# Kernel optimization log

Hardware: AMD Instinct MI355X
Metric: run time of the kernel (lower is better)

## Reference

```python
import jax, jax.numpy as jnp
import numpy as np

NH, HD, WS, LL, SR, HF = 8, 32, 3, 9, 8, 682


def _ln(x, w, b, eps=1e-5):
    m = x.mean(-1, keepdims=True)
    v = ((x - m) ** 2).mean(-1, keepdims=True)
    return (x - m) * jax.lax.rsqrt(v + eps) * w + b


def _l2norm(x, eps=1e-12):
    n = jnp.sqrt(jnp.sum(x * x, axis=-1, keepdims=True))
    return x / jnp.maximum(n, eps)


def setup_inputs() -> dict:
    key = jax.random.key(0)
    ks = jax.random.split(key, 32)
    f32 = jnp.float32
    rn = lambda i, shp, s=0.02: jax.random.normal(ks[i], shp, f32) * s
    B, N, C, T = 8, 3136, 256, 1024
    d = {}
    d['x'] = jax.random.normal(ks[0], (B, N, C), f32)
    d['relative_coords_table'] = jax.random.uniform(ks[1], (T, 2), f32, minval=-1.0, maxval=1.0)
    d['seq_length_scale'] = jnp.ones((1,), f32)
    d['norm1_w'] = jnp.ones((C,), f32); d['norm1_b'] = jnp.zeros((C,), f32)
    d['q_w'] = rn(2, (C, C)); d['q_b'] = rn(3, (C,))
    d['kv_w'] = rn(4, (2 * C, C)); d['kv_b'] = rn(5, (2 * C,))
    d['temperature'] = jnp.full((NH, 1, 1), np.log(np.expm1(1.0 / 0.24)), f32)
    d['query_embedding'] = rn(6, (NH, 1, HD))
    d['relative_pos_bias_local'] = rn(7, (NH, LL), 0.0004)
    d['learnable_tokens'] = rn(8, (NH, HD, LL))
    d['learnable_bias'] = jnp.zeros((NH, 1, LL), f32)
    d['sr_w'] = rn(9, (C, C)); d['sr_b'] = rn(10, (C,))
    d['normp_w'] = jnp.ones((C,), f32); d['normp_b'] = jnp.zeros((C,), f32)
    d['cpb_fc1_w'] = rn(11, (512, 2)); d['cpb_fc1_b'] = rn(12, (512,))
    d['cpb_fc2_w'] = rn(13, (NH, 512)); d['cpb_fc2_b'] = rn(14, (NH,))
    d['proj_w'] = rn(15, (C, C)); d['proj_b'] = rn(16, (C,))
    d['norm2_w'] = jnp.ones((C,), f32); d['norm2_b'] = jnp.zeros((C,), f32)
    d['fc1_w'] = rn(17, (2 * HF, C)); d['fc1_b'] = rn(18, (2 * HF,))
    d['dw_w'] = rn(19, (HF, 1, 3, 3)); d['dw_b'] = rn(20, (HF,))
    d['fc2_w'] = rn(21, (C, HF)); d['fc2_b'] = rn(22, (C,))
    d['relative_pos_index'] = jax.random.randint(ks[23], (N, 49), 0, T)
    d['padding_mask'] = jnp.zeros((N, LL), bool)
    d['H'] = 56
    d['W'] = 56
    return d


def _forward(x, relative_coords_table, seq_length_scale, norm1_w, norm1_b, q_w, q_b, kv_w, kv_b,
             temperature, query_embedding, relative_pos_bias_local, learnable_tokens, learnable_bias,
             sr_w, sr_b, normp_w, normp_b, cpb_fc1_w, cpb_fc1_b, cpb_fc2_w, cpb_fc2_b,
             proj_w, proj_b, norm2_w, norm2_b, fc1_w, fc1_b, dw_w, dw_b, fc2_w, fc2_b,
             relative_pos_index, padding_mask, H, W):
    B, N, C = x.shape
    pH, pW = H // SR, W // SR
    pl = pH * pW
    xn = _ln(x, norm1_w, norm1_b)
    # queries: [B, nh, N, hd], cosine-normalized
    q = (xn @ q_w.T + q_b).reshape(B, N, NH, HD).transpose(0, 2, 1, 3)
    q_norm = _l2norm(q)
    q_scaled = (q_norm + query_embedding) * jax.nn.softplus(temperature) * seq_length_scale
    # local keys/values via unfold (3x3 windows, zero-padded)
    kv = xn @ kv_w.T + kv_b                                   # [B, N, 2C]
    k_l, v_l = jnp.split(kv, 2, axis=-1)
    k_l = _l2norm(k_l.reshape(B, N, NH, HD)).reshape(B, N, C)
    kvl = jnp.concatenate([k_l, v_l], -1).transpose(0, 2, 1).reshape(B, 2 * C, H, W)
    pad = WS // 2
    kvp = jnp.pad(kvl, ((0, 0), (0, 0), (pad, pad), (pad, pad)))
    wins = jnp.stack([kvp[:, :, i:i + H, j:j + W] for i in range(WS) for j in range(WS)], axis=2)
    wins = wins.reshape(B, 2 * NH, HD, LL, N).transpose(0, 1, 4, 2, 3)  # [B, 2nh, N, hd, ll]
    k_loc, v_loc = jnp.split(wins, 2, axis=1)
    attn_local = jnp.einsum('bhnd,bhndl->bhnl', q_scaled, k_loc) + relative_pos_bias_local[None, :, None, :]
    attn_local = jnp.where(padding_mask[None, None], -jnp.inf, attn_local)
    # pooled global branch
    x_ = xn.transpose(0, 2, 1).reshape(B, C, H, W)
    x_ = jax.nn.gelu(jnp.einsum('oc,bchw->bohw', sr_w, x_) + sr_b[None, :, None, None], approximate=False)
    x_ = x_.reshape(B, C, pH, SR, pW, SR).mean(axis=(3, 5))  # adaptive avg pool
    x_ = _ln(x_.reshape(B, C, pl).transpose(0, 2, 1), normp_w, normp_b)
    kvp2 = (x_ @ kv_w.T + kv_b).reshape(B, pl, 2 * NH, HD).transpose(0, 2, 1, 3)
    k_pool, v_pool = jnp.split(kvp2, 2, axis=1)               # [B, nh, pl, hd]
    cpb = jax.nn.relu(relative_coords_table @ cpb_fc1_w.T + cpb_fc1_b) @ cpb_fc2_w.T + cpb_fc2_b
    pool_bias = cpb.T[:, relative_pos_index.reshape(-1)].reshape(NH, N, pl)
    attn_pool = q_scaled @ _l2norm(k_pool).transpose(0, 1, 3, 2) + pool_bias[None]
    # joint softmax over local + pool scores
    attn = jax.nn.softmax(jnp.concatenate([attn_local, attn_pool], -1), axis=-1)
    a_loc, a_pool = attn[..., :LL], attn[..., LL:]
    x_local = jnp.einsum('bhnl,bhndl->bhnd',
                         jnp.einsum('bhnd,hdl->bhnl', q_norm, learnable_tokens) + learnable_bias[None] + a_loc,
                         v_loc)
    x_pool = a_pool @ v_pool
    out = (x_local + x_pool).transpose(0, 2, 1, 3).reshape(B, N, C)
    x = x + (out @ proj_w.T + proj_b)
    # ConvolutionalGLU MLP
    xn2 = _ln(x, norm2_w, norm2_b)
    h = xn2 @ fc1_w.T + fc1_b
    h1, v = jnp.split(h, 2, -1)
    hc = h1.transpose(0, 2, 1).reshape(B, HF, H, W)
    hc = jax.lax.conv_general_dilated(hc, dw_w, (1, 1), 'SAME', feature_group_count=HF,
                                      dimension_numbers=('NCHW', 'OIHW', 'NCHW')) + dw_b[None, :, None, None]
    h1 = hc.reshape(B, HF, N).transpose(0, 2, 1)
    h = jax.nn.gelu(h1, approximate=False) * v
    return x + (h @ fc2_w.T + fc2_b)


def reference(x, relative_coords_table, seq_length_scale, norm1_w, norm1_b, q_w, q_b, kv_w, kv_b,
              temperature, query_embedding, relative_pos_bias_local, learnable_tokens, learnable_bias,
              sr_w, sr_b, normp_w, normp_b, cpb_fc1_w, cpb_fc1_b, cpb_fc2_w, cpb_fc2_b,
              proj_w, proj_b, norm2_w, norm2_b, fc1_w, fc1_b, dw_w, dw_b, fc2_w, fc2_b,
              relative_pos_index, padding_mask, H, W):
    return _forward(x, relative_coords_table, seq_length_scale, norm1_w, norm1_b, q_w, q_b, kv_w, kv_b,
                    temperature, query_embedding, relative_pos_bias_local, learnable_tokens, learnable_bias,
                    sr_w, sr_b, normp_w, normp_b, cpb_fc1_w, cpb_fc1_b, cpb_fc2_w, cpb_fc2_b,
                    proj_w, proj_b, norm2_w, norm2_b, fc1_w, fc1_b, dw_w, dw_b, fc2_w, fc2_b,
                    relative_pos_index, padding_mask, H, W)
```

## Files before the change

kernel.cpp:

```cpp
#include <hip/hip_runtime.h>
#include <math.h>

#define B_   8
#define N_   3136
#define C_   256
#define NH_  8
#define HD_  32
#define LL_  9
#define PL_  49
#define HF_  682
#define HH   56
#define WW   56
#define MROWS (B_*N_)
#define HGLD  704
#define F2LD  704
#define HBLD  1368

typedef short          bf16x8 __attribute__((ext_vector_type(8)));
typedef unsigned short u16x8  __attribute__((ext_vector_type(8)));
typedef float          f32x4  __attribute__((ext_vector_type(4)));
typedef unsigned short u16;

static __device__ __forceinline__ float gelu_f(float x){ return 0.5f*x*(1.0f+erff(x*0.70710678118654752f)); }
static __device__ __forceinline__ u16 f2bf(float f){
  union { float f; unsigned u; } x; x.f = f;
  unsigned r = (x.u + 0x7FFFu + ((x.u >> 16) & 1u)) >> 16;
  return (u16)r;
}
static __device__ __forceinline__ float b2f(u16 u){
  union { unsigned u; float f; } x; x.u = ((unsigned)u) << 16;
  return x.f;
}
static __device__ __forceinline__ void gld_lds16(const u16* g, u16* l){
  __builtin_amdgcn_global_load_lds((const __attribute__((address_space(1))) void*)g,
                                   (__attribute__((address_space(3))) void*)l, 16, 0, 0);
}
static __device__ __forceinline__ float rsum32(float v){
  #pragma unroll
  for (int m=16;m>0;m>>=1) v += __shfl_xor(v,m,32);
  return v;
}
static __device__ __forceinline__ float rsum64(float v){
  #pragma unroll
  for (int m=32;m>0;m>>=1) v += __shfl_xor(v,m,64);
  return v;
}

__global__ __launch_bounds__(256) void cvt4_kernel(const float* __restrict__ src,
                                                   u16* __restrict__ dst, int n4){
  int i = blockIdx.x*256 + threadIdx.x;
  if (i >= n4) return;
  float4 v = *(const float4*)(src + (size_t)i*4);
  ushort4 o; o.x=f2bf(v.x); o.y=f2bf(v.y); o.z=f2bf(v.z); o.w=f2bf(v.w);
  *(ushort4*)(dst + (size_t)i*4) = o;
}
__global__ __launch_bounds__(256) void cvt_pad_kernel(const float* __restrict__ src,
                                                      u16* __restrict__ dst,
                                                      int rows, int K, int ldw){
  int i = blockIdx.x*256 + threadIdx.x;
  if (i >= rows*ldw) return;
  int r = i/ldw, k = i - r*ldw;
  dst[i] = (k < K) ? f2bf(src[(size_t)r*K + k]) : (u16)0;
}

__global__ __launch_bounds__(256) void ln_kernel(const float* __restrict__ in,
                                                 const float* __restrict__ w,
                                                 const float* __restrict__ bsh,
                                                 u16* __restrict__ out){
  int row = blockIdx.x, tid = threadIdx.x;
  float v = in[(size_t)row*C_+tid];
  float s = rsum64(v), q = rsum64(v*v);
  __shared__ float s1[4], s2[4];
  if ((tid&63)==0){ s1[tid>>6]=s; s2[tid>>6]=q; }
  __syncthreads();
  float ts=s1[0]+s1[1]+s1[2]+s1[3];
  float tq=s2[0]+s2[1]+s2[2]+s2[3];
  float m = ts*(1.0f/C_);
  float var = tq*(1.0f/C_)-m*m;
  float inv = rsqrtf(var+1e-5f);
  out[(size_t)row*C_+tid] = f2bf((v-m)*inv*w[tid]+bsh[tid]);
}

template<int ACT, int RES, int OUTBF>
__global__ __launch_bounds__(256) void gemm64b(const u16* __restrict__ A, int lda,
                                               const u16* __restrict__ W, int ldw,
                                               const float* __restrict__ bias,
                                               const float* __restrict__ res,
                                               void* __restrict__ outv,
                                               int M, int Nt, int K){
  constexpr int LDT = 40;
  __shared__ u16 As[64*LDT];
  __shared__ u16 Bs[64*LDT];
  int tid = threadIdx.x, lane = tid & 63;
  int wave = tid >> 6;
  int m0 = blockIdx.x*64, n0 = blockIdx.y*64;
  int wm = (wave>>1)*32, wn = (wave&1)*32;
  f32x4 acc[2][2];
  #pragma unroll
  for (int i=0;i<2;i++)
    #pragma unroll
    for (int j=0;j<2;j++) acc[i][j] = (f32x4){0.f,0.f,0.f,0.f};

  const int Kt = (K + 31) & ~31;
  const int l15 = lane & 15, quad = lane >> 4;
  int r  = tid >> 2;
  int c8 = (tid & 3) * 8;

  for (int k0=0; k0<Kt; k0+=32){
    int gk = k0 + c8;
    u16x8 av = (u16x8){0,0,0,0,0,0,0,0};
    if (m0 + r < M && gk + 8 <= lda)
      av = *(const u16x8*)(A + (size_t)(m0+r)*lda + gk);
    *(u16x8*)(&As[r*LDT + c8]) = av;
    u16x8 bv = (u16x8){0,0,0,0,0,0,0,0};
    if (n0 + r < Nt && gk + 8 <= ldw)
      bv = *(const u16x8*)(W + (size_t)(n0+r)*ldw + gk);
    *(u16x8*)(&Bs[r*LDT + c8]) = bv;
    __syncthreads();
    bf16x8 af[2], bfr[2];
    #pragma unroll
    for (int mi=0;mi<2;mi++)
      af[mi] = *(bf16x8*)(&As[(wm + mi*16 + l15)*LDT + quad*8]);
    #pragma unroll
    for (int nj=0;nj<2;nj++)
      bfr[nj] = *(bf16x8*)(&Bs[(wn + nj*16 + l15)*LDT + quad*8]);
    #pragma unroll
    for (int mi=0;mi<2;mi++)
      #pragma unroll
      for (int nj=0;nj<2;nj++)
        acc[mi][nj] = __builtin_amdgcn_mfma_f32_16x16x32_bf16(af[mi], bfr[nj], acc[mi][nj], 0,0,0);
    __syncthreads();
  }
  int rbase = quad*4;
  #pragma unroll
  for (int nj=0;nj<2;nj++){
    int gc = n0 + wn + nj*16 + l15;
    if (gc >= Nt) continue;
    float bv = bias[gc];
    #pragma unroll
    for (int mi=0;mi<2;mi++){
      #pragma unroll
      for (int reg=0;reg<4;reg++){
        int gr = m0 + wm + mi*16 + rbase + reg;
        if (gr >= M) continue;
        float v = acc[mi][nj][reg] + bv;
        if (ACT==1) v = gelu_f(v);
        if (RES)   v += res[(size_t)gr*Nt + gc];
        if (OUTBF) ((u16*)outv)[(size_t)gr*Nt + gc] = f2bf(v);
        else       ((float*)outv)[(size_t)gr*Nt + gc] = v;
      }
    }
  }
}

__global__ __launch_bounds__(256) void gemm128a(const u16* __restrict__ A, int lda,
                                                const u16* __restrict__ W, int ldw,
                                                const float* __restrict__ bias,
                                                u16* __restrict__ out,
                                                int M, int Nt, int K, int ldo){
  __shared__ u16 smem[8704];
  u16* As = smem;
  u16* Bs = smem + 4096;
  int tid = threadIdx.x, lane = tid & 63, wave = tid >> 6;
  int m0 = blockIdx.x*128, n0 = blockIdx.y*128;
  int wm = (wave>>1)*64, wn = (wave&1)*64;
  int l15 = lane & 15, quad = lane >> 4;
  f32x4 acc[4][4];
  #pragma unroll
  for (int i=0;i<4;i++)
    #pragma unroll
    for (int j=0;j<4;j++) acc[i][j] = (f32x4){0.f,0.f,0.f,0.f};

  const int Kt = (K + 31) & ~31;
  const u16* ga = A + (size_t)(m0 + lane)*lda + wave*8;
  const u16* gb = W + (size_t)(n0 + lane)*ldw + wave*8;
  u16* la = As + wave*1024;
  u16* lb = Bs + wave*1024;

  for (int k0=0; k0<Kt; k0+=32){
    gld_lds16(ga + k0,            la);
    gld_lds16(ga + 64*lda + k0,   la + 512);
    gld_lds16(gb + k0,            lb);
    gld_lds16(gb + 64*ldw + k0,   lb + 512);
    __syncthreads();
    bf16x8 af[4], bfr[4];
    #pragma unroll
    for (int mi=0;mi<4;mi++)
      af[mi] = *(bf16x8*)(&As[quad*1024 + (wm + mi*16 + l15)*8]);
    #pragma unroll
    for (int nj=0;nj<4;nj++)
      bfr[nj] = *(bf16x8*)(&Bs[quad*1024 + (wn + nj*16 + l15)*8]);
    #pragma unroll
    for (int mi=0;mi<4;mi++)
      #pragma unroll
      for (int nj=0;nj<4;nj++)
        acc[mi][nj] = __builtin_amdgcn_mfma_f32_16x16x32_bf16(af[mi], bfr[nj], acc[mi][nj], 0,0,0);
    __syncthreads();
  }

  u16* Cs = smem;
  #pragma unroll
  for (int p=0;p<2;p++){
    if (wm == p*64){
      #pragma unroll
      for (int nj=0;nj<4;nj++){
        int cc = wn + nj*16 + l15;
        int gc = n0 + cc;
        float bv = (gc < Nt) ? bias[gc] : 0.f;
        #pragma unroll
        for (int mi=0;mi<4;mi++)
          #pragma unroll
          for (int reg=0;reg<4;reg++){
            int rr = mi*16 + quad*4 + reg;
            Cs[rr*136 + cc] = f2bf(acc[mi][nj][reg] + bv);
          }
      }
    }
    __syncthreads();
    int r = tid >> 2, cb = (tid & 3)*32;
    int gr = m0 + p*64 + r;
    if (gr < M){
      u16* op = out + (size_t)gr*ldo + n0;
      #pragma unroll
      for (int k=0;k<4;k++){
        int c0 = cb + k*8;
        if (n0 + c0 + 8 <= ldo)
          *(u16x8*)(op + c0) = *(u16x8*)&Cs[r*136 + c0];
      }
    }
    __syncthreads();
  }
}

__global__ __launch_bounds__(256) void qpost_kernel(u16* __restrict__ q,
                                                    const float* __restrict__ qe,
                                                    const float* __restrict__ temp,
                                                    const float* __restrict__ sls,
                                                    u16* __restrict__ qs_out){
  int row = blockIdx.x, tid = threadIdx.x, h = tid>>5;
  size_t idx = (size_t)row*C_ + tid;
  float v = b2f(q[idx]);
  float ss = rsum32(v*v);
  float qn = v / fmaxf(sqrtf(ss), 1e-12f);
  q[idx] = f2bf(qn);
  float t  = temp[h];
  float sp = log1pf(expf(t));
  float scale = sp * sls[0];
  qs_out[idx] = f2bf((qn + qe[tid])*scale);
}

__global__ __launch_bounds__(256) void knorm_kernel(u16* __restrict__ kv){
  int row = blockIdx.x, tid = threadIdx.x;
  size_t idx = (size_t)row*512 + tid;
  float v = b2f(kv[idx]);
  float ss = rsum32(v*v);
  kv[idx] = f2bf(v / fmaxf(sqrtf(ss), 1e-12f));
}

__global__ __launch_bounds__(256) void pool_ln_kernel(const u16* __restrict__ xsr,
                                                      const float* __restrict__ w,
                                                      const float* __restrict__ bsh,
                                                      u16* __restrict__ out){
  int blk = blockIdx.x; int b = blk/PL_; int p = blk%PL_;
  int py = p/7, px = p%7;
  int o = threadIdx.x;
  float s = 0.f;
  for (int iy=0;iy<8;iy++){
    const u16* rowp = xsr + ((size_t)(b*N_ + (py*8+iy)*WW + px*8))*C_ + o;
    #pragma unroll
    for (int ix=0;ix<8;ix++) s += b2f(rowp[(size_t)ix*C_]);
  }
  s *= (1.0f/64.0f);
  float su = rsum64(s), sq = rsum64(s*s);
  __shared__ float s1[4], s2[4];
  if ((o&63)==0){ s1[o>>6]=su; s2[o>>6]=sq; }
  __syncthreads();
  float ts=s1[0]+s1[1]+s1[2]+s1[3];
  float tq=s2[0]+s2[1]+s2[2]+s2[3];
  float m = ts*(1.0f/256.0f), var = tq*(1.0f/256.0f)-m*m;
  float inv = rsqrtf(var+1e-5f);
  out[(size_t)blk*C_+o] = f2bf((s-m)*inv*w[o]+bsh[o]);
}

__global__ __launch_bounds__(256) void cpb_kernel(const float* __restrict__ rct,
                                                  const float* __restrict__ w1,
                                                  const float* __restrict__ b1,
                                                  const float* __restrict__ w2,
                                                  const float* __restrict__ b2v,
                                                  float* __restrict__ cpb){
  __shared__ float r[512];
  int t = blockIdx.x, tid = threadIdx.x;
  float c0 = rct[t*2], c1 = rct[t*2+1];
  for (int j=tid;j<512;j+=256){
    float v = c0*w1[j*2] + c1*w1[j*2+1] + b1[j];
    r[j] = fmaxf(v, 0.f);
  }
  __syncthreads();
  int h = tid>>5, lane = tid&31;
  float s = 0.f;
  for (int j=lane;j<512;j+=32) s += r[j]*w2[h*512+j];
  s = rsum32(s);
  if (lane==0) cpb[t*8+h] = s + b2v[h];
}

__global__ __launch_bounds__(256) void attn_local_v3(const u16* __restrict__ qs,
                                                     const u16* __restrict__ kv,
                                                     const float* __restrict__ rpb,
                                                     float* __restrict__ attn){
  int t = threadIdx.x;
  int row = blockIdx.x*32 + (t>>3);
  int h = t & 7;
  int b = row / N_, n = row - b*N_;
  int y = n / WW, x = n - y*WW;
  const u16* qp = qs + (size_t)row*C_ + h*32;
  float q[32];
  #pragma unroll
  for (int j=0;j<4;j++){
    u16x8 v = *(const u16x8*)(qp + j*8);
    #pragma unroll
    for (int e=0;e<8;e++) q[j*8+e] = b2f(v[e]);
  }
  float* arow = attn + ((size_t)row*8 + h)*58;
  #pragma unroll
  for (int l=0;l<9;l++){
    int yy = y + l/3 - 1, xx = x + l%3 - 1;
    float s = 0.f;
    if (yy>=0 && yy<HH && xx>=0 && xx<WW){
      const u16* kp = kv + ((size_t)(b*N_ + yy*WW + xx))*512 + h*32;
      #pragma unroll
      for (int j=0;j<4;j++){
        u16x8 kw = *(const u16x8*)(kp + j*8);
        #pragma unroll
        for (int e=0;e<8;e++) s = fmaf(q[j*8+e], b2f(kw[e]), s);
      }
    }
    arow[l] = s + rpb[h*9+l];
  }
}

__global__ __launch_bounds__(256) void attn_pool_mfma(const u16* __restrict__ qs,
                                                      const u16* __restrict__ kvp2,
                                                      const float* __restrict__ cpb,
                                                      const int* __restrict__ ridx,
                                                      float* __restrict__ attn){
  int tid = threadIdx.x, lane = tid & 63, wave = tid >> 6;
  int l15 = lane & 15, quad = lane >> 4;
  int bh = blockIdx.y, b = bh >> 3, h = bh & 7;
  int n0 = (blockIdx.x*4 + wave)*16;
  bf16x8 af = *(const bf16x8*)(qs + ((size_t)(b*N_ + n0 + l15)*C_ + h*32 + quad*8));
  f32x4 acc[4];
  #pragma unroll
  for (int nj=0;nj<4;nj++){
    int p = nj*16 + l15;
    bf16x8 bfr = (bf16x8){0,0,0,0,0,0,0,0};
    if (p < PL_)
      bfr = *(const bf16x8*)(kvp2 + ((size_t)(b*PL_ + p)*512 + h*32 + quad*8));
    f32x4 z = (f32x4){0.f,0.f,0.f,0.f};
    acc[nj] = __builtin_amdgcn_mfma_f32_16x16x32_bf16(af, bfr, z, 0,0,0);
  }
  #pragma unroll
  for (int nj=0;nj<4;nj++){
    int p = nj*16 + l15;
    if (p >= PL_) continue;
    #pragma unroll
    for (int reg=0;reg<4;reg++){
      int n = n0 + quad*4 + reg;
      float bias = cpb[ridx[(size_t)n*PL_ + p]*8 + h];
      attn[((size_t)(b*N_ + n)*8 + h)*58 + 9 + p] = acc[nj][reg] + bias;
    }
  }
}

__global__ __launch_bounds__(256) void build_w72(const float* __restrict__ lt, u16* __restrict__ w72){
  int r = blockIdx.x, c = threadIdx.x;
  int h = r/9, l = r - h*9;
  w72[(size_t)r*256 + c] = ((c>>5) == h) ? f2bf(lt[((size_t)(h*32 + (c&31)))*9 + l]) : (u16)0;
}
__global__ __launch_bounds__(256) void build_dwwT(const float* __restrict__ dww, float* __restrict__ dwwT){
  int l = blockIdx.x;
  for (int f=threadIdx.x; f<684; f+=256)
    dwwT[(size_t)l*684 + f] = (f < HF_) ? dww[(size_t)f*9 + l] : 0.f;
}

__global__ __launch_bounds__(256) void xout_v4(const float* __restrict__ qlt,
                                               const float* __restrict__ attn,
                                               const u16* __restrict__ kv,
                                               const u16* __restrict__ kvp2,
                                               u16* __restrict__ out){
  __shared__ float coef[4][472];
  int t = threadIdx.x, w = t>>6, l = t&63;
  int row = blockIdx.x*4 + w;
  int b = row / N_, n = row - b*N_;
  int y = n / WW, x = n - y*WW;
  const float* arow = attn + (size_t)row*464;
  for (int i=l; i<464; i+=64) coef[w][i] = arow[i];
  __syncthreads();
  int h = l>>3, k = l&7;
  float* ch = &coef[w][h*58];
  float e[8];
  float mx = -1e30f;
  #pragma unroll
  for (int i=0;i<8;i++){
    int j = k + i*8;
    e[i] = (j<58) ? ch[j] : -1e30f;
    mx = fmaxf(mx, e[i]);
  }
  mx = fmaxf(mx, __shfl_xor(mx,1,64));
  mx = fmaxf(mx, __shfl_xor(mx,2,64));
  mx = fmaxf(mx, __shfl_xor(mx,4,64));
  float s = 0.f;
  #pragma unroll
  for (int i=0;i<8;i++){
    int j = k + i*8;
    if (j<58){ e[i] = expf(e[i]-mx); s += e[i]; }
  }
  s += __shfl_xor(s,1,64);
  s += __shfl_xor(s,2,64);
  s += __shfl_xor(s,4,64);
  float inv = 1.f/s;
  #pragma unroll
  for (int i=0;i<8;i++){
    int j = k + i*8;
    if (j<58){
      float v = e[i]*inv;
      if (j<9) v += qlt[(size_t)row*72 + h*9 + j];
      ch[j] = v;
    }
  }
  __syncthreads();
  int c = l*4;
  float a0=0.f, a1=0.f, a2=0.f, a3=0.f;
  #pragma unroll
  for (int lw=0; lw<9; lw++){
    int yy = y + lw/3 - 1, xx = x + lw%3 - 1;
    if (yy>=0 && yy<HH && xx>=0 && xx<WW){
      ushort4 vv = *(const ushort4*)(kv + ((size_t)(b*N_ + yy*WW + xx))*512 + 256 + c);
      float cf = ch[lw];
      a0 = fmaf(cf, b2f(vv.x), a0);
      a1 = fmaf(cf, b2f(vv.y), a1);
      a2 = fmaf(cf, b2f(vv.z), a2);
      a3 = fmaf(cf, b2f(vv.w), a3);
    }
  }
  const u16* pb = kvp2 + (size_t)b*PL_*512 + 256 + c;
  #pragma unroll 7
  for (int p=0;p<49;p++){
    ushort4 vv = *(const ushort4*)(pb + (size_t)p*512);
    float cf = ch[9+p];
    a0 = fmaf(cf, b2f(vv.x), a0);
    a1 = fmaf(cf, b2f(vv.y), a1);
    a2 = fmaf(cf, b2f(vv.z), a2);
    a3 = fmaf(cf, b2f(vv.w), a3);
  }
  ushort4 o; o.x=f2bf(a0); o.y=f2bf(a1); o.z=f2bf(a2); o.w=f2bf(a3);
  *(ushort4*)(out + (size_t)row*C_ + c) = o;
}

__global__ __launch_bounds__(256) void dwconv_v4(const u16* __restrict__ hsrc,
                                                 const float* __restrict__ dwwT,
                                                 const float* __restrict__ dwb,
                                                 u16* __restrict__ hg){
  int b = blockIdx.x;
  int idx = blockIdx.y*256 + threadIdx.x;
  if (idx >= N_*86) return;
  int n = idx/86, g = idx - n*86;
  int pix = b*N_ + n;
  int y = n / WW, x = n - y*WW;
  const u16* hb = hsrc + (size_t)b*N_*HBLD;
  if (g < 85){
    int f = g*8;
    float s[8];
    #pragma unroll
    for (int e=0;e<8;e++) s[e] = dwb[f+e];
    #pragma unroll
    for (int l=0;l<9;l++){
      int yy = y + l/3 - 1, xx = x + l%3 - 1;
      if (yy>=0 && yy<HH && xx>=0 && xx<WW){
        u16x8 hv = *(const u16x8*)(hb + (size_t)(yy*WW+xx)*HBLD + f);
        const float* wv = dwwT + (size_t)l*684 + f;
        #pragma unroll
        for (int e=0;e<8;e++) s[e] = fmaf(b2f(hv[e]), wv[e], s[e]);
      }
    }
    const u16* vp = hsrc + (size_t)pix*HBLD + HF_ + f;
    u16 ov[8];
    #pragma unroll
    for (int e=0;e<8;e++) ov[e] = f2bf(gelu_f(s[e]) * b2f(vp[e]));
    *(u16x8*)(hg + (size_t)pix*HGLD + f) = *(u16x8*)ov;
  } else {
    float r[2];
    #pragma unroll
    for (int c=0;c<2;c++){
      int ff = 680 + c;
      float s = dwb[ff];
      #pragma unroll
      for (int l=0;l<9;l++){
        int yy = y + l/3 - 1, xx = x + l%3 - 1;
        if (yy>=0 && yy<HH && xx>=0 && xx<WW)
          s += b2f(hb[(size_t)(yy*WW+xx)*HBLD + ff]) * dwwT[(size_t)l*684 + ff];
      }
      r[c] = gelu_f(s) * b2f(hsrc[(size_t)pix*HBLD + HF_ + ff]);
    }
    u16* hp = hg + (size_t)pix*HGLD;
    ushort4 o1; o1.x = f2bf(r[0]); o1.y = f2bf(r[1]); o1.z = 0; o1.w = 0;
    *(ushort4*)(hp + 680) = o1;
    ushort4 z4 = {0,0,0,0};
    *(ushort4*)(hp + 684) = z4;
    *(ushort4*)(hp + 688) = z4;
    *(ushort4*)(hp + 692) = z4;
    *(ushort4*)(hp + 696) = z4;
    *(ushort4*)(hp + 700) = z4;
  }
}

extern "C" void kernel_launch(void* const* d_in, const int* in_sizes, int n_in,
                              void* d_out, int out_size, void* d_ws, size_t ws_size,
                              hipStream_t stream) {
  const float* x    = (const float*)d_in[0];
  const float* rct  = (const float*)d_in[1];
  const float* sls  = (const float*)d_in[2];
  const float* n1w  = (const float*)d_in[3];
  const float* n1b  = (const float*)d_in[4];
  const float* q_w  = (const float*)d_in[5];
  const float* q_b  = (const float*)d_in[6];
  const float* kv_w = (const float*)d_in[7];
  const float* kv_b = (const float*)d_in[8];
  const float* temp = (const float*)d_in[9];
  const float* qe   = (const float*)d_in[10];
  const float* rpb  = (const float*)d_in[11];
  const float* lt   = (const float*)d_in[12];
  const float* lb   = (const float*)d_in[13];
  const float* sr_w = (const float*)d_in[14];
  const float* sr_b = (const float*)d_in[15];
  const float* npw  = (const float*)d_in[16];
  const float* npb  = (const float*)d_in[17];
  const float* c1w  = (const float*)d_in[18];
  const float* c1b  = (const float*)d_in[19];
  const float* c2w  = (const float*)d_in[20];
  const float* c2b  = (const float*)d_in[21];
  const float* pw   = (const float*)d_in[22];
  const float* pb   = (const float*)d_in[23];
  const float* n2w  = (const float*)d_in[24];
  const float* n2b  = (const float*)d_in[25];
  const float* f1w  = (const float*)d_in[26];
  const float* f1b  = (const float*)d_in[27];
  const float* dww  = (const float*)d_in[28];
  const float* dwb  = (const float*)d_in[29];
  const float* f2w  = (const float*)d_in[30];
  const float* f2bb = (const float*)d_in[31];
  const int*  ridx  = (const int*)d_in[32];
  float* outp = (float*)d_out;

  char* ws = (char*)d_ws;
  constexpr size_t SZ_BNC2 = (size_t)MROWS*C_*2;
  constexpr size_t SZ_KV2  = (size_t)MROWS*512*2;
  constexpr size_t SZ_ATTN = (size_t)MROWS*464*4;
  size_t o_xn   = 0;
  size_t o_qn   = o_xn   + SZ_BNC2;
  size_t o_qs   = o_qn   + SZ_BNC2;
  size_t o_kv   = o_qs   + SZ_BNC2;
  size_t o_attn = o_kv   + SZ_KV2;
  size_t o_xsr  = o_attn + SZ_ATTN;
  size_t o_xpln = o_xsr  + SZ_BNC2;
  size_t o_kvp2 = o_xpln + (size_t)B_*PL_*C_*2;
  size_t o_cpb  = o_kvp2 + (size_t)B_*PL_*512*2;
  size_t o_outb = o_cpb  + (size_t)1024*8*4;
  size_t o_x2   = o_outb + SZ_BNC2;
  size_t o_qlt  = o_x2   + (size_t)MROWS*C_*4;
  size_t o_wq   = o_qlt  + (size_t)MROWS*72*4;
  size_t o_wkv  = o_wq   + (size_t)65536*2;
  size_t o_wsr  = o_wkv  + (size_t)131072*2;
  size_t o_wp   = o_wsr  + (size_t)65536*2;
  size_t o_wf1  = o_wp   + (size_t)65536*2;
  size_t o_wf2  = o_wf1  + (size_t)349184*2;
  size_t o_w72  = o_wf2  + (size_t)256*F2LD*2;
  size_t o_dwwT = o_w72  + (size_t)72*256*2;
  size_t o_h    = o_kv;
  size_t o_hg   = 0;

  u16*   xn   = (u16*)(ws + o_xn);
  u16*   qbuf = (u16*)(ws + o_qn);
  u16*   qsc  = (u16*)(ws + o_qs);
  u16*   kv   = (u16*)(ws + o_kv);
  float* attn = (float*)(ws + o_attn);
  u16*   xsr  = (u16*)(ws + o_xsr);
  u16*   xpln = (u16*)(ws + o_xpln);
  u16*   kvp2 = (u16*)(ws + o_kvp2);
  float* cpb  = (float*)(ws + o_cpb);
  u16*   outb = (u16*)(ws + o_outb);
  float* x2   = (float*)(ws + o_x2);
  float* qlt  = (float*)(ws + o_qlt);
  u16*   wq   = (u16*)(ws + o_wq);
  u16*   wkv  = (u16*)(ws + o_wkv);
  u16*   wsr  = (u16*)(ws + o_wsr);
  u16*   wp   = (u16*)(ws + o_wp);
  u16*   wf1  = (u16*)(ws + o_wf1);
  u16*   wf2  = (u16*)(ws + o_wf2);
  u16*   w72  = (u16*)(ws + o_w72);
  float* dwwT = (float*)(ws + o_dwwT);
  u16*   hbuf = (u16*)(ws + o_h);
  u16*   hg   = (u16*)(ws + o_hg);

  cvt4_kernel<<<(65536/4+255)/256, 256, 0, stream>>>(q_w,  wq,  65536/4);
  cvt4_kernel<<<(131072/4+255)/256,256, 0, stream>>>(kv_w, wkv, 131072/4);
  cvt4_kernel<<<(65536/4+255)/256, 256, 0, stream>>>(sr_w, wsr, 65536/4);
  cvt4_kernel<<<(65536/4+255)/256, 256, 0, stream>>>(pw,   wp,  65536/4);
  cvt4_kernel<<<(349184/4+255)/256,256, 0, stream>>>(f1w,  wf1, 349184/4);
  cvt_pad_kernel<<<(256*F2LD+255)/256, 256, 0, stream>>>(f2w, wf2, 256, HF_, F2LD);
  build_w72<<<72, 256, 0, stream>>>(lt, w72);
  build_dwwT<<<9, 256, 0, stream>>>(dww, dwwT);

  ln_kernel<<<MROWS, 256, 0, stream>>>(x, n1w, n1b, xn);
  gemm64b<0,0,1><<<dim3(392,4), 256, 0, stream>>>(xn, C_, wq, C_, q_b, nullptr, qbuf, MROWS, 256, 256);
  gemm64b<0,0,1><<<dim3(392,8), 256, 0, stream>>>(xn, C_, wkv, C_, kv_b, nullptr, kv, MROWS, 512, 256);
  qpost_kernel<<<MROWS, 256, 0, stream>>>(qbuf, qe, temp, sls, qsc);
  knorm_kernel<<<MROWS, 256, 0, stream>>>(kv);
  gemm64b<1,0,1><<<dim3(392,4), 256, 0, stream>>>(xn, C_, wsr, C_, sr_b, nullptr, xsr, MROWS, 256, 256);
  pool_ln_kernel<<<B_*PL_, 256, 0, stream>>>(xsr, npw, npb, xpln);
  gemm64b<0,0,1><<<dim3(7,8), 256, 0, stream>>>(xpln, C_, wkv, C_, kv_b, nullptr, kvp2, B_*PL_, 512, 256);
  knorm_kernel<<<B_*PL_, 256, 0, stream>>>(kvp2);
  cpb_kernel<<<1024, 256, 0, stream>>>(rct, c1w, c1b, c2w, c2b, cpb);
  gemm64b<0,0,0><<<dim3(392,2), 256, 0, stream>>>(qbuf, C_, w72, C_, lb, nullptr, qlt, MROWS, 72, 256);
  attn_local_v3<<<MROWS/32, 256, 0, stream>>>(qsc, kv, rpb, attn);
  attn_pool_mfma<<<dim3(49,64), 256, 0, stream>>>(qsc, kvp2, cpb, ridx, attn);
  xout_v4<<<MROWS/4, 256, 0, stream>>>(qlt, attn, kv, kvp2, outb);
  gemm64b<0,1,0><<<dim3(392,4), 256, 0, stream>>>(outb, C_, wp, C_, pb, x, x2, MROWS, 256, 256);
  ln_kernel<<<MROWS, 256, 0, stream>>>(x2, n2w, n2b, xn);
  gemm128a<<<dim3(196,11), 256, 0, stream>>>(xn, C_, wf1, C_, f1b, hbuf, MROWS, 1364, 256, HBLD);
  dwconv_v4<<<dim3(8, (N_*86+255)/256), 256, 0, stream>>>(hbuf, dwwT, dwb, hg);
  gemm64b<0,1,0><<<dim3(392,4), 256, 0, stream>>>(hg, HGLD, wf2, F2LD, f2bb, x2, outp, MROWS, 256, HF_);
}
```

Before: 604.7 us.

## Add full-K resident GEMM and fuse q/kv/sr projections into one launch

Adds a new 128x128-tile GEMM kernel for K=256. It stages the whole A tile (all 8 K-slices, 64KB LDS) in one shot, and the B fragments are loaded straight from global into registers and double-buffered across K steps, so the per-K-step barriers go away. The q, kv and sr (with GELU) projections now share one launch indexed by blockIdx.y, so LN output tiles are reused across them. The proj and fc1 GEMMs also move to this kernel, with the fc1 weights row-padded to 1408 so B loads stay in bounds. The cost is heavy LDS use (occupancy bounded at 2 blocks) and uncoalesced-ish direct global B loads.

```diff
diff --git a/kernel.cpp b/kernel.cpp
--- a/kernel.cpp
+++ b/kernel.cpp
@@ -61,6 +61,14 @@
   if (i >= rows*ldw) return;
   int r = i/ldw, k = i - r*ldw;
   dst[i] = (k < K) ? f2bf(src[(size_t)r*K + k]) : (u16)0;
+}
+__global__ __launch_bounds__(256) void cvt_rowpad_kernel(const float* __restrict__ src,
+                                                         u16* __restrict__ dst,
+                                                         int rows, int srcRows, int K){
+  int i = blockIdx.x*256 + threadIdx.x;
+  if (i >= rows*K) return;
+  int r = i/K;
+  dst[i] = (r < srcRows) ? f2bf(src[i]) : (u16)0;
 }
 
 __global__ __launch_bounds__(256) void ln_kernel(const float* __restrict__ in,
@@ -153,82 +161,129 @@
   }
 }
 
-__global__ __launch_bounds__(256) void gemm128a(const u16* __restrict__ A, int lda,
-                                                const u16* __restrict__ W, int ldw,
-                                                const float* __restrict__ bias,
-                                                u16* __restrict__ out,
-                                                int M, int Nt, int K, int ldo){
-  __shared__ u16 smem[8704];
-  u16* As = smem;
-  u16* Bs = smem + 4096;
+template<int EPI>
+__global__ __launch_bounds__(256,2) void gemmfk(const u16* __restrict__ A,
+                                                const u16* __restrict__ W0,
+                                                const u16* __restrict__ W1,
+                                                const u16* __restrict__ W2,
+                                                const float* __restrict__ b0,
+                                                const float* __restrict__ b1,
+                                                const float* __restrict__ b2,
+                                                const float* __restrict__ res,
+                                                void* __restrict__ o0,
+                                                void* __restrict__ o1,
+                                                void* __restrict__ o2,
+                                                int Nt, int ldo){
+  __shared__ u16 smem[32768];
   int tid = threadIdx.x, lane = tid & 63, wave = tid >> 6;
-  int m0 = blockIdx.x*128, n0 = blockIdx.y*128;
+  int l15 = lane & 15, quad = lane >> 4;
   int wm = (wave>>1)*64, wn = (wave&1)*64;
-  int l15 = lane & 15, quad = lane >> 4;
+  int m0 = blockIdx.x*128, y = blockIdx.y;
+
+  const u16* Wp; const float* bp; u16* dstb = nullptr; int dld = 0, dcol0 = 0; bool act = false;
+  if (EPI==2){
+    if (y < 2){      Wp = W0 + (size_t)y*128*C_;     bp = b0 + y*128;     dstb = (u16*)o0; dld = 256; dcol0 = y*128; }
+    else if (y < 6){ Wp = W1 + (size_t)(y-2)*128*C_; bp = b1 + (y-2)*128; dstb = (u16*)o1; dld = 512; dcol0 = (y-2)*128; }
+    else {           Wp = W2 + (size_t)(y-6)*128*C_; bp = b2 + (y-6)*128; dstb = (u16*)o2; dld = 256; dcol0 = (y-6)*128; act = true; }
+  } else {
+    Wp = W0 + (size_t)y*128*C_; bp = b0; dstb = (u16*)o0; dld = ldo; dcol0 = y*128;
+  }
+
+  const u16* ga = A + (size_t)(m0 + lane)*C_ + wave*8;
+  u16* la = smem + wave*1024;
+  #pragma unroll
+  for (int k=0;k<8;k++){
+    gld_lds16(ga + k*32,                  la + k*4096);
+    gld_lds16(ga + (size_t)64*C_ + k*32,  la + k*4096 + 512);
+  }
+  const u16* gb = Wp + (size_t)(wn + l15)*C_ + quad*8;
+  bf16x8 bc[4];
+  #pragma unroll
+  for (int nj=0;nj<4;nj++) bc[nj] = *(const bf16x8*)(gb + (size_t)nj*16*C_);
+
+  asm volatile("s_waitcnt vmcnt(0)" ::: "memory");
+  __builtin_amdgcn_s_barrier();
+  asm volatile("" ::: "memory");
+
   f32x4 acc[4][4];
   #pragma unroll
   for (int i=0;i<4;i++)
     #pragma unroll
     for (int j=0;j<4;j++) acc[i][j] = (f32x4){0.f,0.f,0.f,0.f};
 
-  const int Kt = (K + 31) & ~31;
-  const u16* ga = A + (size_t)(m0 + lane)*lda + wave*8;
-  const u16* gb = W + (size_t)(n0 + lane)*ldw + wave*8;
-  u16* la = As + wave*1024;
-  u16* lb = Bs + wave*1024;
-
-  for (int k0=0; k0<Kt; k0+=32){
-    gld_lds16(ga + k0,            la);
-    gld_lds16(ga + 64*lda + k0,   la + 512);
-    gld_lds16(gb + k0,            lb);
-    gld_lds16(gb + 64*ldw + k0,   lb + 512);
+  #pragma unroll
+  for (int k=0;k<8;k++){
+    bf16x8 bn[4];
+    if (k < 7){
+      #pragma unroll
+      for (int nj=0;nj<4;nj++) bn[nj] = *(const bf16x8*)(gb + (size_t)nj*16*C_ + (k+1)*32);
+    }
+    bf16x8 af[4];
+    #pragma unroll
+    for (int mi=0;mi<4;mi++)
+      af[mi] = *(bf16x8*)(&smem[k*4096 + quad*1024 + (wm + mi*16 + l15)*8]);
+    #pragma unroll
+    for (int mi=0;mi<4;mi++)
+      #pragma unroll
+      for (int nj=0;nj<4;nj++)
+        acc[mi][nj] = __builtin_amdgcn_mfma_f32_16x16x32_bf16(af[mi], bc[nj], acc[mi][nj], 0,0,0);
+    if (k < 7){
+      #pragma unroll
+      for (int nj=0;nj<4;nj++) bc[nj] = bn[nj];
+    }
+  }
+
+  if (EPI==0 || EPI==2){
     __syncthreads();
-    bf16x8 af[4], bfr[4];
-    #pragma unroll
-    for (int mi=0;mi<4;mi++)
-      af[mi] = *(bf16x8*)(&As[quad*1024 + (wm + mi*16 + l15)*8]);
-    #pragma unroll
-    for (int nj=0;nj<4;nj++)
-      bfr[nj] = *(bf16x8*)(&Bs[quad*1024 + (wn + nj*16 + l15)*8]);
-    #pragma unroll
-    for (int mi=0;mi<4;mi++)
-      #pragma unroll
-      for (int nj=0;nj<4;nj++)
-        acc[mi][nj] = __builtin_amdgcn_mfma_f32_16x16x32_bf16(af[mi], bfr[nj], acc[mi][nj], 0,0,0);
-    __syncthreads();
-  }
-
-  u16* Cs = smem;
-  #pragma unroll
-  for (int p=0;p<2;p++){
-    if (wm == p*64){
-      #pragma unroll
-      for (int nj=0;nj<4;nj++){
-        int cc = wn + nj*16 + l15;
-        int gc = n0 + cc;
-        float bv = (gc < Nt) ? bias[gc] : 0.f;
+    u16* Cs = smem;
+    #pragma unroll
+    for (int p=0;p<2;p++){
+      if (wm == p*64){
         #pragma unroll
-        for (int mi=0;mi<4;mi++)
+        for (int nj=0;nj<4;nj++){
+          int cc = wn + nj*16 + l15;
+          float bv;
+          if (EPI==0){ int gc = dcol0 + cc; bv = (gc < Nt) ? bp[gc] : 0.f; }
+          else       { bv = bp[cc]; }
           #pragma unroll
-          for (int reg=0;reg<4;reg++){
-            int rr = mi*16 + quad*4 + reg;
-            Cs[rr*136 + cc] = f2bf(acc[mi][nj][reg] + bv);
+          for (int mi=0;mi<4;mi++){
+            #pragma unroll
+            for (int reg=0;reg<4;reg++){
+              int rr = mi*16 + quad*4 + reg;
+              float v = acc[mi][nj][reg] + bv;
+              if (act) v = gelu_f(v);
+              Cs[rr*136 + cc] = f2bf(v);
+            }
           }
+        }
       }
-    }
-    __syncthreads();
-    int r = tid >> 2, cb = (tid & 3)*32;
-    int gr = m0 + p*64 + r;
-    if (gr < M){
-      u16* op = out + (size_t)gr*ldo + n0;
-      #pragma unroll
-      for (int k=0;k<4;k++){
-        int c0 = cb + k*8;
-        if (n0 + c0 + 8 <= ldo)
-          *(u16x8*)(op + c0) = *(u16x8*)&Cs[r*136 + c0];
+      __syncthreads();
+      int r = tid >> 2, cb = (tid & 3)*32;
+      int gr = m0 + p*64 + r;
+      u16* op = dstb + (size_t)gr*dld + dcol0;
+      #pragma unroll
+      for (int kk=0;kk<4;kk++){
+        int c0 = cb + kk*8;
+        bool ok = (EPI==0) ? (dcol0 + c0 + 8 <= ldo) : true;
+        if (ok) *(u16x8*)(op + c0) = *(u16x8*)&Cs[r*136 + c0];
       }
-    }
-    __syncthreads();
+      __syncthreads();
+    }
+  } else {
+    float* of = (float*)o0;
+    #pragma unroll
+    for (int nj=0;nj<4;nj++){
+      int gc = dcol0 + wn + nj*16 + l15;
+      float bv = bp[gc];
+      #pragma unroll
+      for (int mi=0;mi<4;mi++){
+        #pragma unroll
+        for (int reg=0;reg<4;reg++){
+          int gr = m0 + wm + mi*16 + quad*4 + reg;
+          of[(size_t)gr*256 + gc] = acc[mi][nj][reg] + bv + res[(size_t)gr*256 + gc];
+        }
+      }
+    }
   }
 }
 
@@ -572,7 +627,7 @@
   size_t o_wsr  = o_wkv  + (size_t)131072*2;
   size_t o_wp   = o_wsr  + (size_t)65536*2;
   size_t o_wf1  = o_wp   + (size_t)65536*2;
-  size_t o_wf2  = o_wf1  + (size_t)349184*2;
+  size_t o_wf2  = o_wf1  + (size_t)360448*2;
   size_t o_w72  = o_wf2  + (size_t)256*F2LD*2;
   size_t o_dwwT = o_w72  + (size_t)72*256*2;
   size_t o_h    = o_kv;
@@ -605,17 +660,16 @@
   cvt4_kernel<<<(131072/4+255)/256,256, 0, stream>>>(kv_w, wkv, 131072/4);
   cvt4_kernel<<<(65536/4+255)/256, 256, 0, stream>>>(sr_w, wsr, 65536/4);
   cvt4_kernel<<<(65536/4+255)/256, 256, 0, stream>>>(pw,   wp,  65536/4);
-  cvt4_kernel<<<(349184/4+255)/256,256, 0, stream>>>(f1w,  wf1, 349184/4);
+  cvt_rowpad_kernel<<<(360448+255)/256, 256, 0, stream>>>(f1w, wf1, 1408, 1364, 256);
   cvt_pad_kernel<<<(256*F2LD+255)/256, 256, 0, stream>>>(f2w, wf2, 256, HF_, F2LD);
   build_w72<<<72, 256, 0, stream>>>(lt, w72);
   build_dwwT<<<9, 256, 0, stream>>>(dww, dwwT);
 
   ln_kernel<<<MROWS, 256, 0, stream>>>(x, n1w, n1b, xn);
-  gemm64b<0,0,1><<<dim3(392,4), 256, 0, stream>>>(xn, C_, wq, C_, q_b, nullptr, qbuf, MROWS, 256, 256);
-  gemm64b<0,0,1><<<dim3(392,8), 256, 0, stream>>>(xn, C_, wkv, C_, kv_b, nullptr, kv, MROWS, 512, 256);
+  gemmfk<2><<<dim3(196,8), 256, 0, stream>>>(xn, wq, wkv, wsr, q_b, kv_b, sr_b,
+                                             nullptr, qbuf, kv, xsr, 1024, 0);
   qpost_kernel<<<MROWS, 256, 0, stream>>>(qbuf, qe, temp, sls, qsc);
   knorm_kernel<<<MROWS, 256, 0, stream>>>(kv);
-  gemm64b<1,0,1><<<dim3(392,4), 256, 0, stream>>>(xn, C_, wsr, C_, sr_b, nullptr, xsr, MROWS, 256, 256);
   pool_ln_kernel<<<B_*PL_, 256, 0, stream>>>(xsr, npw, npb, xpln);
   gemm64b<0,0,1><<<dim3(7,8), 256, 0, stream>>>(xpln, C_, wkv, C_, kv_b, nullptr, kvp2, B_*PL_, 512, 256);
   knorm_kernel<<<B_*PL_, 256, 0, stream>>>(kvp2);
@@ -624,9 +678,11 @@
   attn_local_v3<<<MROWS/32, 256, 0, stream>>>(qsc, kv, rpb, attn);
   attn_pool_mfma<<<dim3(49,64), 256, 0, stream>>>(qsc, kvp2, cpb, ridx, attn);
   xout_v4<<<MROWS/4, 256, 0, stream>>>(qlt, attn, kv, kvp2, outb);
-  gemm64b<0,1,0><<<dim3(392,4), 256, 0, stream>>>(outb, C_, wp, C_, pb, x, x2, MROWS, 256, 256);
+  gemmfk<1><<<dim3(196,2), 256, 0, stream>>>(outb, wp, nullptr, nullptr, pb, nullptr, nullptr,
+                                             x, x2, nullptr, nullptr, 256, 256);
   ln_kernel<<<MROWS, 256, 0, stream>>>(x2, n2w, n2b, xn);
-  gemm128a<<<dim3(196,11), 256, 0, stream>>>(xn, C_, wf1, C_, f1b, hbuf, MROWS, 1364, 256, HBLD);
+  gemmfk<0><<<dim3(196,11), 256, 0, stream>>>(xn, wf1, nullptr, nullptr, f1b, nullptr, nullptr,
+                                              nullptr, hbuf, nullptr, nullptr, 1364, HBLD);
   dwconv_v4<<<dim3(8, (N_*86+255)/256), 256, 0, stream>>>(hbuf, dwwT, dwb, hg);
   gemm64b<0,1,0><<<dim3(392,4), 256, 0, stream>>>(hg, HGLD, wf2, F2LD, f2bb, x2, outp, MROWS, 256, HF_);
 }
```

Measured after the change: 655.0 us. 8.3% more time.

## Fuse weight conversions, q/kv/sr GEMMs, and q/k normalization into fewer kernels

Applied to the files above, without the earlier changes.

Eight small weight-conversion and setup kernels become one multi-segment kernel selected by blockIdx.y. The q, kv and sr projection GEMMs that share the normalized input become a single launch with 16 column tiles, so the input is read in one pass and launch count drops. The key L2-normalization is folded into the q post-processing kernel. The new fused GEMM is a simpler 64x64 tile kernel without the prior kernel's pipelining, which could lower per-tile efficiency. The wf1 buffer is also padded to 1408 rows with zeros.

```diff
diff --git a/kernel.cpp b/kernel.cpp
--- a/kernel.cpp
+++ b/kernel.cpp
@@ -46,21 +46,65 @@
   return v;
 }
 
-__global__ __launch_bounds__(256) void cvt4_kernel(const float* __restrict__ src,
-                                                   u16* __restrict__ dst, int n4){
-  int i = blockIdx.x*256 + threadIdx.x;
-  if (i >= n4) return;
-  float4 v = *(const float4*)(src + (size_t)i*4);
-  ushort4 o; o.x=f2bf(v.x); o.y=f2bf(v.y); o.z=f2bf(v.z); o.w=f2bf(v.w);
-  *(ushort4*)(dst + (size_t)i*4) = o;
-}
-__global__ __launch_bounds__(256) void cvt_pad_kernel(const float* __restrict__ src,
-                                                      u16* __restrict__ dst,
-                                                      int rows, int K, int ldw){
-  int i = blockIdx.x*256 + threadIdx.x;
-  if (i >= rows*ldw) return;
-  int r = i/ldw, k = i - r*ldw;
-  dst[i] = (k < K) ? f2bf(src[(size_t)r*K + k]) : (u16)0;
+__global__ __launch_bounds__(256) void cvt_all(const float* __restrict__ q_w,
+                                               const float* __restrict__ kv_w,
+                                               const float* __restrict__ sr_w,
+                                               const float* __restrict__ pw,
+                                               const float* __restrict__ f1w,
+                                               const float* __restrict__ f2w,
+                                               const float* __restrict__ lt,
+                                               const float* __restrict__ dww,
+                                               u16* __restrict__ wq,
+                                               u16* __restrict__ wkv,
+                                               u16* __restrict__ wsr,
+                                               u16* __restrict__ wp,
+                                               u16* __restrict__ wf1,
+                                               u16* __restrict__ wf2,
+                                               u16* __restrict__ w72,
+                                               float* __restrict__ dwwT){
+  int t = blockIdx.x*256 + threadIdx.x;
+  int seg = blockIdx.y;
+  const int NT = 64*256;
+  if (seg == 0){
+    float4 v = *(const float4*)(q_w + (size_t)t*4);
+    ushort4 o; o.x=f2bf(v.x); o.y=f2bf(v.y); o.z=f2bf(v.z); o.w=f2bf(v.w);
+    *(ushort4*)(wq + (size_t)t*4) = o;
+  } else if (seg == 1){
+    for (int i=t; i<32768; i+=NT){
+      float4 v = *(const float4*)(kv_w + (size_t)i*4);
+      ushort4 o; o.x=f2bf(v.x); o.y=f2bf(v.y); o.z=f2bf(v.z); o.w=f2bf(v.w);
+      *(ushort4*)(wkv + (size_t)i*4) = o;
+    }
+  } else if (seg == 2){
+    float4 v = *(const float4*)(sr_w + (size_t)t*4);
+    ushort4 o; o.x=f2bf(v.x); o.y=f2bf(v.y); o.z=f2bf(v.z); o.w=f2bf(v.w);
+    *(ushort4*)(wsr + (size_t)t*4) = o;
+  } else if (seg == 3){
+    float4 v = *(const float4*)(pw + (size_t)t*4);
+    ushort4 o; o.x=f2bf(v.x); o.y=f2bf(v.y); o.z=f2bf(v.z); o.w=f2bf(v.w);
+    *(ushort4*)(wp + (size_t)t*4) = o;
+  } else if (seg == 4){
+    for (int i=t; i<360448; i+=NT){
+      int r = i >> 8;
+      wf1[i] = (r < 1364) ? f2bf(f1w[i]) : (u16)0;
+    }
+  } else if (seg == 5){
+    for (int i=t; i<256*F2LD; i+=NT){
+      int r = i/F2LD, k = i - r*F2LD;
+      wf2[i] = (k < HF_) ? f2bf(f2w[(size_t)r*HF_ + k]) : (u16)0;
+    }
+  } else if (seg == 6){
+    for (int i=t; i<72*256; i+=NT){
+      int r = i >> 8, c = i & 255;
+      int h = r/9, l = r - h*9;
+      w72[i] = ((c>>5) == h) ? f2bf(lt[((size_t)(h*32 + (c&31)))*9 + l]) : (u16)0;
+    }
+  } else {
+    for (int i=t; i<9*684; i+=NT){
+      int l = i/684, f = i - l*684;
+      dwwT[i] = (f < HF_) ? dww[(size_t)f*9 + l] : 0.f;
+    }
+  }
 }
 
 __global__ __launch_bounds__(256) void ln_kernel(const float* __restrict__ in,
@@ -153,6 +197,75 @@
   }
 }
 
+__global__ __launch_bounds__(256) void gemm64f(const u16* __restrict__ A,
+                                               const u16* __restrict__ W0,
+                                               const u16* __restrict__ W1,
+                                               const u16* __restrict__ W2,
+                                               const float* __restrict__ b0,
+                                               const float* __restrict__ b1,
+                                               const float* __restrict__ b2,
+                                               u16* __restrict__ o0,
+                                               u16* __restrict__ o1,
+                                               u16* __restrict__ o2){
+  constexpr int LDT = 40;
+  __shared__ u16 As[64*LDT];
+  __shared__ u16 Bs[64*LDT];
+  int tid = threadIdx.x, lane = tid & 63;
+  int wave = tid >> 6;
+  int m0 = blockIdx.x*64, y = blockIdx.y;
+  const u16* Wp; const float* bp; u16* dst; int dld, dcol0; bool act = false;
+  if (y < 4)      { Wp = W0 + (size_t)y*64*C_;      bp = b0 + y*64;      dst = o0; dld = 256; dcol0 = y*64; }
+  else if (y < 12){ Wp = W1 + (size_t)(y-4)*64*C_;  bp = b1 + (y-4)*64;  dst = o1; dld = 512; dcol0 = (y-4)*64; }
+  else            { Wp = W2 + (size_t)(y-12)*64*C_; bp = b2 + (y-12)*64; dst = o2; dld = 256; dcol0 = (y-12)*64; act = true; }
+  int wm = (wave>>1)*32, wn = (wave&1)*32;
+  f32x4 acc[2][2];
+  #pragma unroll
+  for (int i=0;i<2;i++)
+    #pragma unroll
+    for (int j=0;j<2;j++) acc[i][j] = (f32x4){0.f,0.f,0.f,0.f};
+
+  const int l15 = lane & 15, quad = lane >> 4;
+  int r  = tid >> 2;
+  int c8 = (tid & 3) * 8;
+
+  #pragma unroll 1
+  for (int k0=0; k0<256; k0+=32){
+    int gk = k0 + c8;
+    *(u16x8*)(&As[r*LDT + c8]) = *(const u16x8*)(A  + (size_t)(m0+r)*C_ + gk);
+    *(u16x8*)(&Bs[r*LDT + c8]) = *(const u16x8*)(Wp + (size_t)r*C_ + gk);
+    __syncthreads();
+    bf16x8 af[2], bfr[2];
+    #pragma unroll
+    for (int mi=0;mi<2;mi++)
+      af[mi] = *(bf16x8*)(&As[(wm + mi*16 + l15)*LDT + quad*8]);
+    #pragma unroll
+    for (int nj=0;nj<2;nj++)
+      bfr[nj] = *(bf16x8*)(&Bs[(wn + nj*16 + l15)*LDT + quad*8]);
+    #pragma unroll
+    for (int mi=0;mi<2;mi++)
+      #pragma unroll
+      for (int nj=0;nj<2;nj++)
+        acc[mi][nj] = __builtin_amdgcn_mfma_f32_16x16x32_bf16(af[mi], bfr[nj], acc[mi][nj], 0,0,0);
+    __syncthreads();
+  }
+  int rbase = quad*4;
+  #pragma unroll
+  for (int nj=0;nj<2;nj++){
+    int cc = wn + nj*16 + l15;
+    float bv = bp[cc];
+    #pragma unroll
+    for (int mi=0;mi<2;mi++){
+      #pragma unroll
+      for (int reg=0;reg<4;reg++){
+        int gr = m0 + wm + mi*16 + rbase + reg;
+        float v = acc[mi][nj][reg] + bv;
+        if (act) v = gelu_f(v);
+        dst[(size_t)gr*dld + dcol0 + cc] = f2bf(v);
+      }
+    }
+  }
+}
+
 __global__ __launch_bounds__(256) void gemm128a(const u16* __restrict__ A, int lda,
                                                 const u16* __restrict__ W, int ldw,
                                                 const float* __restrict__ bias,
@@ -232,11 +345,12 @@
   }
 }
 
-__global__ __launch_bounds__(256) void qpost_kernel(u16* __restrict__ q,
-                                                    const float* __restrict__ qe,
-                                                    const float* __restrict__ temp,
-                                                    const float* __restrict__ sls,
-                                                    u16* __restrict__ qs_out){
+__global__ __launch_bounds__(256) void qkpost_kernel(u16* __restrict__ q,
+                                                     const float* __restrict__ qe,
+                                                     const float* __restrict__ temp,
+                                                     const float* __restrict__ sls,
+                                                     u16* __restrict__ qs_out,
+                                                     u16* __restrict__ kv){
   int row = blockIdx.x, tid = threadIdx.x, h = tid>>5;
   size_t idx = (size_t)row*C_ + tid;
   float v = b2f(q[idx]);
@@ -247,6 +361,10 @@
   float sp = log1pf(expf(t));
   float scale = sp * sls[0];
   qs_out[idx] = f2bf((qn + qe[tid])*scale);
+  size_t kidx = (size_t)row*512 + tid;
+  float kvv = b2f(kv[kidx]);
+  float ks = rsum32(kvv*kvv);
+  kv[kidx] = f2bf(kvv / fmaxf(sqrtf(ks), 1e-12f));
 }
 
 __global__ __launch_bounds__(256) void knorm_kernel(u16* __restrict__ kv){
@@ -369,17 +487,6 @@
       attn[((size_t)(b*N_ + n)*8 + h)*58 + 9 + p] = acc[nj][reg] + bias;
     }
   }
-}
-
-__global__ __launch_bounds__(256) void build_w72(const float* __restrict__ lt, u16* __restrict__ w72){
-  int r = blockIdx.x, c = threadIdx.x;
-  int h = r/9, l = r - h*9;
-  w72[(size_t)r*256 + c] = ((c>>5) == h) ? f2bf(lt[((size_t)(h*32 + (c&31)))*9 + l]) : (u16)0;
-}
-__global__ __launch_bounds__(256) void build_dwwT(const float* __restrict__ dww, float* __restrict__ dwwT){
-  int l = blockIdx.x;
-  for (int f=threadIdx.x; f<684; f+=256)
-    dwwT[(size_t)l*684 + f] = (f < HF_) ? dww[(size_t)f*9 + l] : 0.f;
 }
 
 __global__ __launch_bounds__(256) void xout_v4(const float* __restrict__ qlt,
@@ -572,7 +679,7 @@
   size_t o_wsr  = o_wkv  + (size_t)131072*2;
   size_t o_wp   = o_wsr  + (size_t)65536*2;
   size_t o_wf1  = o_wp   + (size_t)65536*2;
-  size_t o_wf2  = o_wf1  + (size_t)349184*2;
+  size_t o_wf2  = o_wf1  + (size_t)360448*2;
   size_t o_w72  = o_wf2  + (size_t)256*F2LD*2;
   size_t o_dwwT = o_w72  + (size_t)72*256*2;
   size_t o_h    = o_kv;
@@ -601,21 +708,12 @@
   u16*   hbuf = (u16*)(ws + o_h);
   u16*   hg   = (u16*)(ws + o_hg);
 
-  cvt4_kernel<<<(65536/4+255)/256, 256, 0, stream>>>(q_w,  wq,  65536/4);
-  cvt4_kernel<<<(131072/4+255)/256,256, 0, stream>>>(kv_w, wkv, 131072/4);
-  cvt4_kernel<<<(65536/4+255)/256, 256, 0, stream>>>(sr_w, wsr, 65536/4);
-  cvt4_kernel<<<(65536/4+255)/256, 256, 0, stream>>>(pw,   wp,  65536/4);
-  cvt4_kernel<<<(349184/4+255)/256,256, 0, stream>>>(f1w,  wf1, 349184/4);
-  cvt_pad_kernel<<<(256*F2LD+255)/256, 256, 0, stream>>>(f2w, wf2, 256, HF_, F2LD);
-  build_w72<<<72, 256, 0, stream>>>(lt, w72);
-  build_dwwT<<<9, 256, 0, stream>>>(dww, dwwT);
-
+  cvt_all<<<dim3(64,8), 256, 0, stream>>>(q_w, kv_w, sr_w, pw, f1w, f2w, lt, dww,
+                                          wq, wkv, wsr, wp, wf1, wf2, w72, dwwT);
   ln_kernel<<<MROWS, 256, 0, stream>>>(x, n1w, n1b, xn);
-  gemm64b<0,0,1><<<dim3(392,4), 256, 0, stream>>>(xn, C_, wq, C_, q_b, nullptr, qbuf, MROWS, 256, 256);
-  gemm64b<0,0,1><<<dim3(392,8), 256, 0, stream>>>(xn, C_, wkv, C_, kv_b, nullptr, kv, MROWS, 512, 256);
-  qpost_kernel<<<MROWS, 256, 0, stream>>>(qbuf, qe, temp, sls, qsc);
-  knorm_kernel<<<MROWS, 256, 0, stream>>>(kv);
-  gemm64b<1,0,1><<<dim3(392,4), 256, 0, stream>>>(xn, C_, wsr, C_, sr_b, nullptr, xsr, MROWS, 256, 256);
+  gemm64f<<<dim3(392,16), 256, 0, stream>>>(xn, wq, wkv, wsr, q_b, kv_b, sr_b,
+                                            qbuf, kv, xsr);
+  qkpost_kernel<<<MROWS, 256, 0, stream>>>(qbuf, qe, temp, sls, qsc, kv);
   pool_ln_kernel<<<B_*PL_, 256, 0, stream>>>(xsr, npw, npb, xpln);
   gemm64b<0,0,1><<<dim3(7,8), 256, 0, stream>>>(xpln, C_, wkv, C_, kv_b, nullptr, kvp2, B_*PL_, 512, 256);
   knorm_kernel<<<B_*PL_, 256, 0, stream>>>(kvp2);
```

New measurement: 571.3 us. -5.5%, faster.
